# Performance work log

Hardware: AMD Instinct MI355X
Metric: run time of the kernel (lower is better)

Reference implementation:

```python
import jax, jax.numpy as jnp
import numpy as np

VOCAB = 40
CHAR_EMB = 32
CELLS = [512, 1024, 2048]
EMB_SIZE = 512


def _gru_cell(x, h, w_ih, w_hh, b_ih, b_hh):
    # torch GRUCell: gates ordered (r, z, n); w_ih: [3H, In], w_hh: [3H, H]
    gi = x @ w_ih.T + b_ih
    gh = h @ w_hh.T + b_hh
    i_r, i_z, i_n = jnp.split(gi, 3, axis=-1)
    h_r, h_z, h_n = jnp.split(gh, 3, axis=-1)
    r = jax.nn.sigmoid(i_r + h_r)
    zg = jax.nn.sigmoid(i_z + h_z)
    n = jnp.tanh(i_n + r * h_n)
    return (1.0 - zg) * n + zg * h


def setup_inputs() -> dict:
    key = jax.random.key(0)
    ks = iter(jax.random.split(key, 32))

    def glorot(k, shape):
        fan = sum(shape)
        return jax.random.normal(k, shape, jnp.float32) * (2.0 / fan) ** 0.5

    inp = {
        "z": jax.random.normal(next(ks), (64, EMB_SIZE), jnp.float32),
        "emb": glorot(next(ks), (VOCAB, CHAR_EMB)),
        "fc_init_w": glorot(next(ks), (sum(CELLS), EMB_SIZE)),
        "fc_init_b": jnp.zeros((sum(CELLS),), jnp.float32),
        "fc_out_w": glorot(next(ks), (VOCAB, CELLS[-1])),
    }
    in_size = CHAR_EMB
    for li, h in enumerate(CELLS):
        inp[f"w_ih{li}"] = glorot(next(ks), (3 * h, in_size))
        inp[f"w_hh{li}"] = glorot(next(ks), (3 * h, h))
        inp[f"b_ih{li}"] = jnp.zeros((3 * h,), jnp.float32)
        inp[f"b_hh{li}"] = jnp.zeros((3 * h,), jnp.float32)
        in_size = h
    inp["max_len"] = 64
    inp["start_token"] = 1
    return inp


def reference(z, emb, fc_init_w, fc_init_b, fc_out_w,
              w_ih0, w_hh0, b_ih0, b_hh0,
              w_ih1, w_hh1, b_ih1, b_hh1,
              w_ih2, w_hh2, b_ih2, b_hh2,
              max_len, start_token):
    batch = z.shape[0]
    init_states = z @ fc_init_w.T + fc_init_b  # [B, sum(CELLS)]
    splits = np.cumsum(CELLS)[:-1].tolist()
    h0, h1, h2 = jnp.split(init_states, splits, axis=1)
    layers = [(w_ih0, w_hh0, b_ih0, b_hh0),
              (w_ih1, w_hh1, b_ih1, b_hh1),
              (w_ih2, w_hh2, b_ih2, b_hh2)]
    dec0 = jnp.full((batch,), start_token, dtype=jnp.int32)

    def step(carry, _):
        (h0, h1, h2), dec_in = carry
        x = emb[dec_in]  # [B, CHAR_EMB]
        hs = []
        for hprev, (wi, wh, bi, bh) in zip((h0, h1, h2), layers):
            hnew = _gru_cell(x, hprev, wi, wh, bi, bh)
            hs.append(hnew)
            x = hnew
        logits = x @ fc_out_w.T  # [B, VOCAB]
        dec = jnp.argmax(logits, axis=-1).astype(jnp.int32)
        return ((hs[0], hs[1], hs[2]), dec), dec

    _, toks = jax.lax.scan(step, ((h0, h1, h2), dec0), None, length=max_len)
    # toks: [max_len, B] -> [B, max_len, 1] to match torch stack of unsqueezed outputs
    return toks.T[:, :, None].astype(jnp.int64)
```

## Files before the change

### kernel.cpp

```cpp
#include <hip/hip_runtime.h>
#include <math.h>


#define BATCH 64

typedef short bf16x8 __attribute__((ext_vector_type(8)));
typedef float f32x4  __attribute__((ext_vector_type(4)));

__device__ __forceinline__ float sigmoid_f(float x) { return 1.0f / (1.0f + expf(-x)); }

__device__ __forceinline__ void fma4(float& a, const float4 w, const float4 x) {
    a = fmaf(w.x, x.x, a); a = fmaf(w.y, x.y, a);
    a = fmaf(w.z, x.z, a); a = fmaf(w.w, x.w, a);
}

__device__ __forceinline__ unsigned short f2bf(float x) {
    unsigned u = __float_as_uint(x);
    return (unsigned short)((u + 0x7fff + ((u >> 16) & 1)) >> 16);
}
__device__ __forceinline__ float bf2f(unsigned short h) {
    return __uint_as_float(((unsigned)h) << 16);
}
__device__ __forceinline__ void split_bf(float v, short& hi, short& lo) {
    unsigned short h = f2bf(v);
    hi = (short)h;
    lo = (short)f2bf(v - bf2f(h));
}

__device__ __forceinline__ void frag_scatter(short* xhi, short* xlo,
                                             int j, int b, float v) {
    short h, l2; split_bf(v, h, l2);
    const int kblk = j >> 5, off = j & 31;
    const int lp = ((off >> 3) << 4) + (b & 15);
    const int ii = off & 7;
    const int nt = b >> 4;
    const size_t idx = (((size_t)kblk * 4 + nt) * 64 + lp) * 8 + ii;
    xhi[idx] = h; xlo[idx] = l2;
}

__global__ __launch_bounds__(256) void init_misc(
    const float* __restrict__ z, float* __restrict__ zT4,
    int* __restrict__ dec, const int* __restrict__ start_tok)
{
    int tid = blockIdx.x * 256 + threadIdx.x;
    int b  = tid >> 7;
    int k4 = tid & 127;
    ((float4*)zT4)[k4 * 64 + b] = ((const float4*)z)[b * 128 + k4];
    if (tid < BATCH) dec[tid] = start_tok[0];
}

__global__ __launch_bounds__(256) void init_hstate(
    const float* __restrict__ zT4, const float* __restrict__ w,
    const float* __restrict__ bias,
    float* __restrict__ h0, float* __restrict__ h1, float* __restrict__ h2)
{
    const int wave = threadIdx.x >> 6;
    const int b    = threadIdx.x & 63;
    const int r    = blockIdx.x * 4 + wave;
    const float4* w4 = (const float4*)(w + (size_t)r * 512);
    const float4* z4 = (const float4*)zT4;
    float acc = 0.f;
#pragma unroll 8
    for (int k = 0; k < 128; ++k) fma4(acc, w4[k], z4[k * 64 + b]);
    acc += bias[r];
    float* dst; int j;
    if (r < 512)       { dst = h0; j = r; }
    else if (r < 1536) { dst = h1; j = r - 512; }
    else               { dst = h2; j = r - 1536; }
    dst[(((j >> 2) * 64 + b) << 2) + (j & 3)] = acc;
}

__global__ __launch_bounds__(256) void initfrag(
    const float* __restrict__ hT4, short* __restrict__ xhi, short* __restrict__ xlo)
{
    const int gid = blockIdx.x * 256 + threadIdx.x;
    const int j = gid >> 6, b = gid & 63;
    const float v = hT4[(((j >> 2) * 64 + b) << 2) + (j & 3)];
    frag_scatter(xhi, xlo, j, b, v);
}

template<int H, int IN>
__device__ __forceinline__ void wtransform_body(
    const float* __restrict__ w_ih, const float* __restrict__ w_hh,
    short* __restrict__ dhi, short* __restrict__ dlo)
{
    constexpr int KB = (IN + H) / 32;
    const int unit = blockIdx.x * 4 + (threadIdx.x >> 6);
    const int l    = threadIdx.x & 63;
    const int mtile = unit / KB, kblk = unit % KB;
    const int row = mtile * 16 + (l & 15);
    const int kk  = kblk * 32 + ((l >> 4) << 3);
    const float* src = (kk < IN) ? (w_ih + (size_t)row * IN + kk)
                                 : (w_hh + (size_t)row * H + (kk - IN));
    const float4 v0 = *(const float4*)src;
    const float4 v1 = *(const float4*)(src + 4);
    const float vv[8] = {v0.x, v0.y, v0.z, v0.w, v1.x, v1.y, v1.z, v1.w};
    short hi[8], lo[8];
#pragma unroll
    for (int i = 0; i < 8; ++i) split_bf(vv[i], hi[i], lo[i]);
    const size_t base = ((size_t)unit * 64 + l) * 8;
    *(bf16x8*)(dhi + base) = *(const bf16x8*)hi;
    *(bf16x8*)(dlo + base) = *(const bf16x8*)lo;
}
__global__ __launch_bounds__(256) void wtrans_l1(
    const float* __restrict__ a, const float* __restrict__ b,
    short* __restrict__ c, short* __restrict__ d)
{ wtransform_body<1024, 512>(a, b, c, d); }
__global__ __launch_bounds__(256) void wtrans_l2(
    const float* __restrict__ a, const float* __restrict__ b,
    short* __restrict__ c, short* __restrict__ d)
{ wtransform_body<2048, 1024>(a, b, c, d); }

template<int H, int IN, int MT>
__device__ __forceinline__ void mfma_gate_body(
    const short* __restrict__ Whi, const short* __restrict__ Wlo,
    const short* __restrict__ XxHi, const short* __restrict__ XxLo,
    const short* __restrict__ XhHi, const short* __restrict__ XhLo,
    float* __restrict__ G)
{
    constexpr int KB  = (IN + H) / 32;
    constexpr int KXB = IN / 32;
    constexpr int GS  = H / 16;
    constexpr int GS2 = GS / MT;
    constexpr int KQ4 = KB / 4;
    constexpr int NG  = KQ4 / 4;

    __shared__ __align__(16) char smem[2 * 2 * 4 * MT * 2 * 512 * 2];
    auto Ast = (short (*)[2][4][MT][2][512])smem;
    auto red = (float (*)[MT][8][64])smem;

    const int tid = threadIdx.x;
    const int wid = tid >> 6;
    const int l   = tid & 63;
    const int nt  = wid & 3;
    const int kh  = wid >> 2;
    const int kq   = blockIdx.x & 1;
    const int rest = blockIdx.x >> 1;
    const int g    = rest / GS2;
    const int jb   = rest % GS2;

    const int kbase = kq * (KB / 2) + kh * KQ4;
    const int pl  = nt & 1;
    const int kl0 = nt >> 1;

    const short* wsrc[MT];
#pragma unroll
    for (int mt = 0; mt < MT; ++mt)
        wsrc[mt] = (pl ? Wlo : Whi)
                 + ((size_t)(g * GS + jb * MT + mt) * KB) * 512;

    f32x4 aXa[MT], aXb[MT], aHa[MT], aHb[MT];
#pragma unroll
    for (int mt = 0; mt < MT; ++mt) {
        aXa[mt] = f32x4{0, 0, 0, 0}; aXb[mt] = f32x4{0, 0, 0, 0};
        aHa[mt] = f32x4{0, 0, 0, 0}; aHb[mt] = f32x4{0, 0, 0, 0};
    }

    auto stage = [&](int buf, int grp) {
        const int kbb = kbase + grp * 4;
#pragma unroll
        for (int u = 0; u < 2 * MT; ++u) {
            const int kloc = kl0 + (u & 1) * 2;
            const int mt   = u >> 1;
            const short* ga = wsrc[mt] + (size_t)(kbb + kloc) * 512 + (size_t)l * 8;
            __builtin_amdgcn_global_load_lds(
                (const __attribute__((address_space(1))) unsigned int*)ga,
                (__attribute__((address_space(3))) unsigned int*)&Ast[buf][kh][kloc][mt][pl][0],
                16, 0, 0);
        }
    };

    auto comp = [&](int buf, const short* bsH, const short* bsL,
                    f32x4 (&A1)[MT], f32x4 (&A2)[MT]) {
#pragma unroll
        for (int i = 0; i < 4; ++i) {
            const size_t bo = (size_t)i * 2048 + (size_t)nt * 512 + (size_t)l * 8;
            const bf16x8 bh = *(const bf16x8*)(bsH + bo);
            const bf16x8 bl = *(const bf16x8*)(bsL + bo);
#pragma unroll
            for (int mt = 0; mt < MT; ++mt) {
                const bf16x8 ah = *(const bf16x8*)&Ast[buf][kh][i][mt][0][(size_t)l * 8];
                const bf16x8 al = *(const bf16x8*)&Ast[buf][kh][i][mt][1][(size_t)l * 8];
                A1[mt] = __builtin_amdgcn_mfma_f32_16x16x32_bf16(ah, bh, A1[mt], 0, 0, 0);
                A2[mt] = __builtin_amdgcn_mfma_f32_16x16x32_bf16(ah, bl, A2[mt], 0, 0, 0);
                A2[mt] = __builtin_amdgcn_mfma_f32_16x16x32_bf16(al, bh, A2[mt], 0, 0, 0);
            }
        }
    };

    stage(0, 0);
    __syncthreads();
#pragma unroll
    for (int grp = 0; grp < NG; ++grp) {
        const int buf = grp & 1;
        if (grp + 1 < NG) stage(buf ^ 1, grp + 1);
        const int kbb = kbase + grp * 4;
        if (kbb < KXB)
            comp(buf, XxHi + (size_t)kbb * 2048, XxLo + (size_t)kbb * 2048, aXa, aXb);
        else
            comp(buf, XhHi + (size_t)(kbb - KXB) * 2048,
                      XhLo + (size_t)(kbb - KXB) * 2048, aHa, aHb);
        __syncthreads();
    }

    float SX[MT][4], SH[MT][4];
#pragma unroll
    for (int mt = 0; mt < MT; ++mt)
#pragma unroll
        for (int t = 0; t < 4; ++t) {
            SX[mt][t] = aXa[mt][t] + aXb[mt][t];
            SH[mt][t] = aHa[mt][t] + aHb[mt][t];
        }

    if (kh == 1) {
#pragma unroll
        for (int mt = 0; mt < MT; ++mt)
#pragma unroll
            for (int t = 0; t < 4; ++t) {
                red[nt][mt][t][l]     = SX[mt][t];
                red[nt][mt][4 + t][l] = SH[mt][t];
            }
    }
    __syncthreads();
    if (kh == 0) {
        const int b = nt * 16 + (l & 15);
#pragma unroll
        for (int mt = 0; mt < MT; ++mt)
#pragma unroll
            for (int t = 0; t < 4; ++t) {
                const float sx = SX[mt][t] + red[nt][mt][t][l];
                const float sh = SH[mt][t] + red[nt][mt][4 + t][l];
                const int j = (jb * MT + mt) * 16 + ((l >> 4) << 2) + t;
                if (g == 0)      G[(size_t)((kq * 4 + 0) * H + j) * 64 + b] = sx + sh;
                else if (g == 1) G[(size_t)((kq * 4 + 1) * H + j) * 64 + b] = sx + sh;
                else {
                    G[(size_t)((kq * 4 + 2) * H + j) * 64 + b] = sx;
                    G[(size_t)((kq * 4 + 3) * H + j) * 64 + b] = sh;
                }
            }
    }
}
__global__ __launch_bounds__(512, 2) void mfma_l1(
    const short* __restrict__ a, const short* __restrict__ b,
    const short* __restrict__ c, const short* __restrict__ d,
    const short* __restrict__ e, const short* __restrict__ f,
    float* __restrict__ g)
{ mfma_gate_body<1024, 512, 1>(a, b, c, d, e, f, g); }
__global__ __launch_bounds__(512, 2) void mfma_l2(
    const short* __restrict__ a, const short* __restrict__ b,
    const short* __restrict__ c, const short* __restrict__ d,
    const short* __restrict__ e, const short* __restrict__ f,
    float* __restrict__ g)
{ mfma_gate_body<2048, 1024, 2>(a, b, c, d, e, f, g); }

template<int H>
__device__ __forceinline__ void comb_body(
    const float* __restrict__ G,
    const float* __restrict__ b_ih, const float* __restrict__ b_hh,
    float* __restrict__ hT4, short* __restrict__ xhi, short* __restrict__ xlo)
{
    const int gid = blockIdx.x * 256 + threadIdx.x;
    const int j = gid >> 6, b = gid & 63;
    const size_t o = (size_t)j * 64 + b;
    const size_t P = (size_t)H * 64;
    const float R  = G[0 * P + o] + G[4 * P + o];
    const float Z  = G[1 * P + o] + G[5 * P + o];
    const float NX = G[2 * P + o] + G[6 * P + o];
    const float NH = G[3 * P + o] + G[7 * P + o];
    const float r  = sigmoid_f(R + b_ih[j] + b_hh[j]);
    const float zg = sigmoid_f(Z + b_ih[H + j] + b_hh[H + j]);
    const float n  = tanhf(NX + b_ih[2 * H + j] + r * (NH + b_hh[2 * H + j]));
    const int idx = (((j >> 2) * 64 + b) << 2) + (j & 3);
    const float hp = hT4[idx];
    const float hn = (1.f - zg) * n + zg * hp;
    hT4[idx] = hn;
    frag_scatter(xhi, xlo, j, b, hn);
}
__global__ __launch_bounds__(256) void comb_l1(
    const float* __restrict__ G, const float* __restrict__ bi,
    const float* __restrict__ bh, float* __restrict__ h,
    short* __restrict__ xh, short* __restrict__ xl)
{ comb_body<1024>(G, bi, bh, h, xh, xl); }
__global__ __launch_bounds__(256) void comb_l2(
    const float* __restrict__ G, const float* __restrict__ bi,
    const float* __restrict__ bh, float* __restrict__ h,
    short* __restrict__ xh, short* __restrict__ xl)
{ comb_body<2048>(G, bi, bh, h, xh, xl); }

template<int IN, int H, int C, bool L0>
__device__ __forceinline__ void gru2_body(
    const float* __restrict__ xT4,
    const float* __restrict__ emb, const int* __restrict__ dec,
    const float* __restrict__ hT4_in, float* __restrict__ hT4_out,
    const float* __restrict__ w_ih, const float* __restrict__ w_hh,
    const float* __restrict__ b_ih, const float* __restrict__ b_hh,
    short* __restrict__ xw_hi, short* __restrict__ xw_lo)
{
    constexpr int Q  = (IN + H) / 4;
    constexpr int QX = IN / 4;
    constexpr int QW = Q / 8;

    const int tid  = threadIdx.x;
    const int wave = tid >> 6;
    const int b    = tid & 63;
    const int j0   = blockIdx.x * C;
    const int q0 = wave * QW;
    const int q1 = q0 + QW;

    float accR[C], accZ[C], accNX[C], accNH[C];
#pragma unroll
    for (int c = 0; c < C; ++c) { accR[c]=0.f; accZ[c]=0.f; accNX[c]=0.f; accNH[c]=0.f; }

    {
        const int xe = (q1 < QX) ? q1 : QX;
        if (q0 < xe) {
            const float4* xsrc;
            if (L0) { xsrc = (const float4*)(emb + dec[b] * 32); }
            else    { xsrc = (const float4*)xT4; }
            for (int q = q0; q < xe; ++q) {
                const float4 x = L0 ? xsrc[q] : xsrc[q * 64 + b];
#pragma unroll
                for (int c = 0; c < C; ++c) {
                    const int j = j0 + c;
                    fma4(accR[c],  *(const float4*)(w_ih + ((size_t)j * IN) + 4*q), x);
                    fma4(accZ[c],  *(const float4*)(w_ih + ((size_t)(j + H) * IN) + 4*q), x);
                    fma4(accNX[c], *(const float4*)(w_ih + ((size_t)(j + 2*H) * IN) + 4*q), x);
                }
            }
        }
    }
    {
        const int hs0 = (q0 > QX) ? q0 : QX;
        if (hs0 < q1) {
            const float4* h4 = (const float4*)hT4_in;
#pragma unroll 2
            for (int q = hs0; q < q1; ++q) {
                const int qh = q - QX;
                const float4 hv = h4[qh * 64 + b];
#pragma unroll
                for (int c = 0; c < C; ++c) {
                    const int j = j0 + c;
                    fma4(accR[c],  *(const float4*)(w_hh + ((size_t)j * H) + 4*qh), hv);
                    fma4(accZ[c],  *(const float4*)(w_hh + ((size_t)(j + H) * H) + 4*qh), hv);
                    fma4(accNH[c], *(const float4*)(w_hh + ((size_t)(j + 2*H) * H) + 4*qh), hv);
                }
            }
        }
    }

    __shared__ float red[8][C][4][64];
#pragma unroll
    for (int c = 0; c < C; ++c) {
        red[wave][c][0][b] = accR[c];
        red[wave][c][1][b] = accZ[c];
        red[wave][c][2][b] = accNX[c];
        red[wave][c][3][b] = accNH[c];
    }
    __syncthreads();

    if (tid < C * 64) {
        const int c  = tid >> 6;
        const int bb = tid & 63;
        float R = 0.f, Z = 0.f, NX = 0.f, NH = 0.f;
#pragma unroll
        for (int w = 0; w < 8; ++w) {
            R += red[w][c][0][bb]; Z += red[w][c][1][bb];
            NX += red[w][c][2][bb]; NH += red[w][c][3][bb];
        }
        const int j = j0 + c;
        const float r  = sigmoid_f(R + b_ih[j]     + b_hh[j]);
        const float zg = sigmoid_f(Z + b_ih[j + H] + b_hh[j + H]);
        const float n  = tanhf(NX + b_ih[j + 2 * H] + r * (NH + b_hh[j + 2 * H]));
        const float hp = hT4_in[(((j >> 2) * 64 + bb) << 2) + (j & 3)];
        const float hn = (1.f - zg) * n + zg * hp;
        hT4_out[(((j >> 2) * 64 + bb) << 2) + (j & 3)] = hn;
        if (xw_hi) frag_scatter(xw_hi, xw_lo, j, bb, hn);
    }
}
__global__ __launch_bounds__(512) void gru_l0(
    const float* __restrict__ emb, const int* __restrict__ dec,
    const float* __restrict__ hin, float* __restrict__ hout,
    const float* __restrict__ wi, const float* __restrict__ wh,
    const float* __restrict__ bi, const float* __restrict__ bh,
    short* __restrict__ xh, short* __restrict__ xl)
{ gru2_body<32, 512, 2, true>(nullptr, emb, dec, hin, hout, wi, wh, bi, bh, xh, xl); }
__global__ __launch_bounds__(512) void gru_fb1(
    const float* __restrict__ x, const float* __restrict__ hin, float* __restrict__ hout,
    const float* __restrict__ wi, const float* __restrict__ wh,
    const float* __restrict__ bi, const float* __restrict__ bh)
{ gru2_body<512, 1024, 4, false>(x, nullptr, nullptr, hin, hout, wi, wh, bi, bh, nullptr, nullptr); }
__global__ __launch_bounds__(512) void gru_fb2(
    const float* __restrict__ x, const float* __restrict__ hin, float* __restrict__ hout,
    const float* __restrict__ wi, const float* __restrict__ wh,
    const float* __restrict__ bi, const float* __restrict__ bh)
{ gru2_body<1024, 2048, 4, false>(x, nullptr, nullptr, hin, hout, wi, wh, bi, bh, nullptr, nullptr); }

__global__ __launch_bounds__(512) void out_k(
    const float* __restrict__ h2T4, const float* __restrict__ w_out,
    int* __restrict__ dec, int* __restrict__ out, int s, int max_len)
{
    __shared__ float hs[2048];
    __shared__ float lg[40];
    const int b    = blockIdx.x;
    const int tid  = threadIdx.x;
    const int wave = tid >> 6;
    const int lane = tid & 63;

    const float4* h4 = (const float4*)h2T4;
    ((float4*)hs)[tid] = h4[tid * 64 + b];
    __syncthreads();

    const float4* hs4 = (const float4*)hs;
#pragma unroll
    for (int v = wave * 5; v < wave * 5 + 5; ++v) {
        const float4* w4 = (const float4*)(w_out + (size_t)v * 2048);
        float acc = 0.f;
#pragma unroll
        for (int it = 0; it < 8; ++it) {
            const int k4 = it * 64 + lane;
            fma4(acc, w4[k4], hs4[k4]);
        }
#pragma unroll
        for (int off = 32; off > 0; off >>= 1)
            acc += __shfl_down(acc, off, 64);
        if (lane == 0) lg[v] = acc;
    }
    __syncthreads();

    if (tid == 0) {
        float best = lg[0];
        int bi = 0;
#pragma unroll
        for (int v = 1; v < 40; ++v) {
            const float val = lg[v];
            if (val > best) { best = val; bi = v; }
        }
        dec[b] = bi;
        out[b * max_len + s] = bi;
    }
}

extern "C" void kernel_launch(void* const* d_in, const int* in_sizes, int n_in,
                              void* d_out, int out_size, void* d_ws, size_t ws_size,
                              hipStream_t stream)
{
    const float* z         = (const float*)d_in[0];
    const float* emb       = (const float*)d_in[1];
    const float* fc_init_w = (const float*)d_in[2];
    const float* fc_init_b = (const float*)d_in[3];
    const float* fc_out_w  = (const float*)d_in[4];
    const float* w_ih0 = (const float*)d_in[5];
    const float* w_hh0 = (const float*)d_in[6];
    const float* b_ih0 = (const float*)d_in[7];
    const float* b_hh0 = (const float*)d_in[8];
    const float* w_ih1 = (const float*)d_in[9];
    const float* w_hh1 = (const float*)d_in[10];
    const float* b_ih1 = (const float*)d_in[11];
    const float* b_hh1 = (const float*)d_in[12];
    const float* w_ih2 = (const float*)d_in[13];
    const float* w_hh2 = (const float*)d_in[14];
    const float* b_ih2 = (const float*)d_in[15];
    const float* b_hh2 = (const float*)d_in[16];
    const int* start_tok = (const int*)d_in[18];

    int* out = (int*)d_out;
    const int max_len = out_size / BATCH;
    char* ws = (char*)d_ws;

    const size_t NEED = 103547136;

    if (ws_size >= NEED) {
        short* Wf1hi = (short*)(ws + 0);
        short* Wf1lo = (short*)(ws + 9437184);
        short* Wf2hi = (short*)(ws + 18874368);
        short* Wf2lo = (short*)(ws + 56623104);
        short* XB0hi = (short*)(ws + 94371840);
        short* XB0lo = (short*)(ws + 94437376);
        short* XB1hi[2] = { (short*)(ws + 94502912), (short*)(ws + 94765056) };
        short* XB1lo[2] = { (short*)(ws + 94633984), (short*)(ws + 94896128) };
        short* XB2hi[2] = { (short*)(ws + 95027200), (short*)(ws + 95551488) };
        short* XB2lo[2] = { (short*)(ws + 95289344), (short*)(ws + 95813632) };
        float* h0a = (float*)(ws + 96075776);
        float* h0b = (float*)(ws + 96206848);
        float* h1  = (float*)(ws + 96337920);
        float* h2  = (float*)(ws + 96600064);
        float* zT4 = (float*)(ws + 97124352);
        float* G1  = (float*)(ws + 97255424);
        float* G2  = (float*)(ws + 99352576);
        int*   dec = (int*)  (ws + 103546880);

        wtrans_l1<<<2304, 256, 0, stream>>>(w_ih1, w_hh1, Wf1hi, Wf1lo);
        wtrans_l2<<<9216, 256, 0, stream>>>(w_ih2, w_hh2, Wf2hi, Wf2lo);
        init_misc<<<32, 256, 0, stream>>>(z, zT4, dec, start_tok);
        init_hstate<<<896, 256, 0, stream>>>(zT4, fc_init_w, fc_init_b, h0a, h1, h2);
        initfrag<<<256, 256, 0, stream>>>(h1, XB1hi[0], XB1lo[0]);
        initfrag<<<512, 256, 0, stream>>>(h2, XB2hi[0], XB2lo[0]);

        for (int s = 0; s < max_len; ++s) {
            const int pi = s & 1, po = pi ^ 1;
            const float* h0i = pi ? h0b : h0a;
            float*       h0o = pi ? h0a : h0b;
            gru_l0<<<256, 512, 0, stream>>>(emb, dec, h0i, h0o,
                                            w_ih0, w_hh0, b_ih0, b_hh0,
                                            XB0hi, XB0lo);
            mfma_l1<<<384, 512, 0, stream>>>(Wf1hi, Wf1lo, XB0hi, XB0lo,
                                             XB1hi[pi], XB1lo[pi], G1);
            comb_l1<<<256, 256, 0, stream>>>(G1, b_ih1, b_hh1, h1,
                                             XB1hi[po], XB1lo[po]);
            mfma_l2<<<384, 512, 0, stream>>>(Wf2hi, Wf2lo, XB1hi[po], XB1lo[po],
                                             XB2hi[pi], XB2lo[pi], G2);
            comb_l2<<<512, 256, 0, stream>>>(G2, b_ih2, b_hh2, h2,
                                             XB2hi[po], XB2lo[po]);
            out_k<<<64, 512, 0, stream>>>(h2, fc_out_w, dec, out, s, max_len);
        }
    } else {
        float* zT4    = (float*)(ws + 0);
        float* h0b2[2] = { (float*)(ws + 131072), (float*)(ws + 262144) };
        float* h1b2[2] = { (float*)(ws + 393216), (float*)(ws + 655360) };
        float* h2b2[2] = { (float*)(ws + 917504), (float*)(ws + 1441792) };
        int*   dec    = (int*)(ws + 1966080);

        init_misc<<<32, 256, 0, stream>>>(z, zT4, dec, start_tok);
        init_hstate<<<896, 256, 0, stream>>>(zT4, fc_init_w, fc_init_b,
                                             h0b2[0], h1b2[0], h2b2[0]);
        for (int s = 0; s < max_len; ++s) {
            const int pi = s & 1, po = pi ^ 1;
            gru_l0<<<256, 512, 0, stream>>>(emb, dec, h0b2[pi], h0b2[po],
                                            w_ih0, w_hh0, b_ih0, b_hh0,
                                            nullptr, nullptr);
            gru_fb1<<<256, 512, 0, stream>>>(h0b2[po], h1b2[pi], h1b2[po],
                                             w_ih1, w_hh1, b_ih1, b_hh1);
            gru_fb2<<<512, 512, 0, stream>>>(h1b2[po], h2b2[pi], h2b2[po],
                                             w_ih2, w_hh2, b_ih2, b_hh2);
            out_k<<<64, 512, 0, stream>>>(h2b2[po], fc_out_w, dec, out, s, max_len);
        }
    }
}
```

Measured before the change: 3.186 ms.

## Fuse layer-2 GRU gate combine into the output projection kernel

Removes the separate comb_l2 launch on the MFMA path and folds the layer-2 gate combine, hidden-state update and bf16 hi/lo fragment scatter into the output/argmax kernel, which now runs one block per batch row. This saves one kernel launch and a global round trip of h2 per step. In exchange the combine work is spread over only 64 blocks instead of 512, and each block reads gate values with a batch-strided pattern that may coalesce poorly.

```diff
diff --git a/kernel.cpp b/kernel.cpp
--- a/kernel.cpp
+++ b/kernel.cpp
@@ -5,6 +5,7 @@
 #define BATCH 64
 
 typedef short bf16x8 __attribute__((ext_vector_type(8)));
+typedef short bf16x4 __attribute__((ext_vector_type(4)));
 typedef float f32x4  __attribute__((ext_vector_type(4)));
 
 __device__ __forceinline__ float sigmoid_f(float x) { return 1.0f / (1.0f + expf(-x)); }
@@ -281,11 +282,6 @@
     const float* __restrict__ bh, float* __restrict__ h,
     short* __restrict__ xh, short* __restrict__ xl)
 { comb_body<1024>(G, bi, bh, h, xh, xl); }
-__global__ __launch_bounds__(256) void comb_l2(
-    const float* __restrict__ G, const float* __restrict__ bi,
-    const float* __restrict__ bh, float* __restrict__ h,
-    short* __restrict__ xh, short* __restrict__ xl)
-{ comb_body<2048>(G, bi, bh, h, xh, xl); }
 
 template<int IN, int H, int C, bool L0>
 __device__ __forceinline__ void gru2_body(
@@ -395,7 +391,86 @@
     const float* __restrict__ bi, const float* __restrict__ bh)
 { gru2_body<1024, 2048, 4, false>(x, nullptr, nullptr, hin, hout, wi, wh, bi, bh, nullptr, nullptr); }
 
-__global__ __launch_bounds__(512) void out_k(
+__global__ __launch_bounds__(512) void out_comb_k(
+    const float* __restrict__ G,
+    const float* __restrict__ b_ih, const float* __restrict__ b_hh,
+    float* __restrict__ hT4, short* __restrict__ xhi, short* __restrict__ xlo,
+    const float* __restrict__ w_out,
+    int* __restrict__ dec, int* __restrict__ out, int s, int max_len)
+{
+    constexpr int H = 2048;
+    __shared__ float hs[2048];
+    __shared__ float lg[40];
+    const int b    = blockIdx.x;
+    const int tid  = threadIdx.x;
+    const int wave = tid >> 6;
+    const int lane = tid & 63;
+    const size_t P = (size_t)H * 64;
+
+    const int j0 = tid * 4;
+    float hv[4];
+#pragma unroll
+    for (int jj = 0; jj < 4; ++jj) {
+        const int j = j0 + jj;
+        const size_t o = (size_t)j * 64 + b;
+        const float R  = G[0 * P + o] + G[4 * P + o];
+        const float Z  = G[1 * P + o] + G[5 * P + o];
+        const float NX = G[2 * P + o] + G[6 * P + o];
+        const float NH = G[3 * P + o] + G[7 * P + o];
+        const float r  = sigmoid_f(R + b_ih[j] + b_hh[j]);
+        const float zg = sigmoid_f(Z + b_ih[H + j] + b_hh[H + j]);
+        const float n  = tanhf(NX + b_ih[2 * H + j] + r * (NH + b_hh[2 * H + j]));
+        const float hp = hT4[(tid * 64 + b) * 4 + jj];
+        const float hn = (1.f - zg) * n + zg * hp;
+        hv[jj] = hn;
+        hs[j] = hn;
+    }
+    ((float4*)hT4)[tid * 64 + b] = make_float4(hv[0], hv[1], hv[2], hv[3]);
+    {
+        short hh[4], ll[4];
+#pragma unroll
+        for (int jj = 0; jj < 4; ++jj) split_bf(hv[jj], hh[jj], ll[jj]);
+        const int kblk = j0 >> 5, off = j0 & 31;
+        const int lp = ((off >> 3) << 4) + (b & 15);
+        const int ii = off & 7;
+        const int nt = b >> 4;
+        const size_t idx = (((size_t)kblk * 4 + nt) * 64 + lp) * 8 + ii;
+        *(bf16x4*)&xhi[idx] = bf16x4{hh[0], hh[1], hh[2], hh[3]};
+        *(bf16x4*)&xlo[idx] = bf16x4{ll[0], ll[1], ll[2], ll[3]};
+    }
+    __syncthreads();
+
+    const float4* hs4 = (const float4*)hs;
+#pragma unroll
+    for (int v = wave * 5; v < wave * 5 + 5; ++v) {
+        const float4* w4 = (const float4*)(w_out + (size_t)v * 2048);
+        float acc = 0.f;
+#pragma unroll
+        for (int it = 0; it < 8; ++it) {
+            const int k4 = it * 64 + lane;
+            fma4(acc, w4[k4], hs4[k4]);
+        }
+#pragma unroll
+        for (int off = 32; off > 0; off >>= 1)
+            acc += __shfl_down(acc, off, 64);
+        if (lane == 0) lg[v] = acc;
+    }
+    __syncthreads();
+
+    if (tid == 0) {
+        float best = lg[0];
+        int bi = 0;
+#pragma unroll
+        for (int v = 1; v < 40; ++v) {
+            const float val = lg[v];
+            if (val > best) { best = val; bi = v; }
+        }
+        dec[b] = bi;
+        out[b * max_len + s] = bi;
+    }
+}
+
+__global__ __launch_bounds__(512) void out_fb(
     const float* __restrict__ h2T4, const float* __restrict__ w_out,
     int* __restrict__ dec, int* __restrict__ out, int s, int max_len)
 {
@@ -509,9 +584,9 @@
                                              XB1hi[po], XB1lo[po]);
             mfma_l2<<<384, 512, 0, stream>>>(Wf2hi, Wf2lo, XB1hi[po], XB1lo[po],
                                              XB2hi[pi], XB2lo[pi], G2);
-            comb_l2<<<512, 256, 0, stream>>>(G2, b_ih2, b_hh2, h2,
-                                             XB2hi[po], XB2lo[po]);
-            out_k<<<64, 512, 0, stream>>>(h2, fc_out_w, dec, out, s, max_len);
+            out_comb_k<<<64, 512, 0, stream>>>(G2, b_ih2, b_hh2, h2,
+                                               XB2hi[po], XB2lo[po],
+                                               fc_out_w, dec, out, s, max_len);
         }
     } else {
         float* zT4    = (float*)(ws + 0);
@@ -532,7 +607,7 @@
                                              w_ih1, w_hh1, b_ih1, b_hh1);
             gru_fb2<<<512, 512, 0, stream>>>(h1b2[po], h2b2[pi], h2b2[po],
                                              w_ih2, w_hh2, b_ih2, b_hh2);
-            out_k<<<64, 512, 0, stream>>>(h2b2[po], fc_out_w, dec, out, s, max_len);
-        }
-    }
-}
+            out_fb<<<64, 512, 0, stream>>>(h2b2[po], fc_out_w, dec, out, s, max_len);
+        }
+    }
+}
```

Result: slower. 4.123 ms (+29.4%).
